# Performance work log

Measured on AMD Instinct MI355X. Metric: run time of the kernel, lower is better.

The kernel has to match this reference:

```python
import jax, jax.numpy as jnp
import numpy as np

D_MODEL = 768
N_HEADS = 12
HEAD_DIM = D_MODEL // N_HEADS
B, L = 2, 4096


def setup_inputs() -> dict:
    key = jax.random.key(0)
    ks = jax.random.split(key, 11)
    s = 0.02
    inp = {
        "q": jax.random.normal(ks[0], (B, L, D_MODEL), jnp.float32),
        "k": jax.random.normal(ks[1], (B, L, D_MODEL), jnp.float32),
        "v": jax.random.normal(ks[2], (B, L, D_MODEL), jnp.float32),
        # causal mask: True = masked (matches torch masked_fill semantics)
        "mask": jnp.triu(jnp.ones((L, L), bool), k=1)[None, None, :, :],
        "wq": jax.random.normal(ks[3], (D_MODEL, D_MODEL), jnp.float32) * s,
        "bq": jnp.zeros((D_MODEL,), jnp.float32),
        "wk": jax.random.normal(ks[4], (D_MODEL, D_MODEL), jnp.float32) * s,
        "bk": jnp.zeros((D_MODEL,), jnp.float32),
        "wv": jax.random.normal(ks[5], (D_MODEL, D_MODEL), jnp.float32) * s,
        "bv": jnp.zeros((D_MODEL,), jnp.float32),
        "wo": jax.random.normal(ks[6], (D_MODEL, D_MODEL), jnp.float32) * s,
        "bo": jnp.zeros((D_MODEL,), jnp.float32),
    }
    return inp


def reference(q, k, v, mask, wq, bq, wk, bk, wv, bv, wo, bo):
    Bs, Ls, Ds = q.shape

    def split_heads(x):  # [B,L,D] -> [B,H,L,hd]
        return x.reshape(Bs, -1, N_HEADS, HEAD_DIM).transpose(0, 2, 1, 3)

    qh = split_heads(q @ wq.T + bq)
    kh = split_heads(k @ wk.T + bk)
    vh = split_heads(v @ wv.T + bv)

    scores = jnp.einsum("bhqd,bhkd->bhqk", qh, kh) / jnp.sqrt(
        jnp.asarray(HEAD_DIM, qh.dtype)
    )
    scores = jnp.where(mask, -jnp.inf, scores)
    attn = jax.nn.softmax(scores, axis=-1)
    out = jnp.einsum("bhqk,bhkd->bhqd", attn, vh)  # [B,H,L,hd]
    out = out.transpose(0, 2, 1, 3).reshape(Bs, Ls, Ds)
    return out @ wo.T + bo
```

## Files before the change

### kernel.cpp

```cpp
#include <hip/hip_runtime.h>
#include <hip/hip_bf16.h>
#include <stdint.h>

#define DM 768
#define NH 12
#define HD 64
#define BB 2
#define LL 4096
#define BH (BB*NH)
#define ML (BB*LL)

typedef short bf16x8 __attribute__((ext_vector_type(8)));
typedef short bf16x4 __attribute__((ext_vector_type(4)));
typedef float f32x4 __attribute__((ext_vector_type(4)));

#define LOG2E 1.4426950408889634f

__device__ inline short f2b(float f) {
  __hip_bfloat16 h = __float2bfloat16(f);
  return *reinterpret_cast<short*>(&h);
}

__device__ inline void gll16(const void* g, void* l) {
  __builtin_amdgcn_global_load_lds(
      (const __attribute__((address_space(1))) unsigned int*)g,
      (__attribute__((address_space(3))) unsigned int*)l, 16, 0, 0);
}

__global__ __launch_bounds__(256) void convx_kernel(
    const float* __restrict__ src, short* __restrict__ dst)
{
  size_t i = ((size_t)blockIdx.x * 256 + threadIdx.x) * 8;
  float4 a = *(const float4*)(src + i);
  float4 b = *(const float4*)(src + i + 4);
  bf16x8 r = {f2b(a.x), f2b(a.y), f2b(a.z), f2b(a.w),
              f2b(b.x), f2b(b.y), f2b(b.z), f2b(b.w)};
  *(bf16x8*)(dst + i) = r;
}

__global__ __launch_bounds__(256) void convx3_kernel(
    const float* __restrict__ s0, const float* __restrict__ s1,
    const float* __restrict__ s2, short* __restrict__ d0,
    short* __restrict__ d1, short* __restrict__ d2)
{
  const float* src = blockIdx.y == 0 ? s0 : (blockIdx.y == 1 ? s1 : s2);
  short*       dst = blockIdx.y == 0 ? d0 : (blockIdx.y == 1 ? d1 : d2);
  size_t i = ((size_t)blockIdx.x * 256 + threadIdx.x) * 8;
  float4 a = *(const float4*)(src + i);
  float4 b = *(const float4*)(src + i + 4);
  bf16x8 r = {f2b(a.x), f2b(a.y), f2b(a.z), f2b(a.w),
              f2b(b.x), f2b(b.y), f2b(b.z), f2b(b.w)};
  *(bf16x8*)(dst + i) = r;
}

__global__ __launch_bounds__(256) void convw_kernel(
    const float* __restrict__ w0, const float* __restrict__ w1,
    const float* __restrict__ w2, const float* __restrict__ w3,
    short* __restrict__ o0, short* __restrict__ o1,
    short* __restrict__ o2, short* __restrict__ o3)
{
  const float* src; short* dst;
  switch (blockIdx.y) {
    case 0: src = w0; dst = o0; break;
    case 1: src = w1; dst = o1; break;
    case 2: src = w2; dst = o2; break;
    default: src = w3; dst = o3; break;
  }
  size_t i = ((size_t)blockIdx.x * 256 + threadIdx.x) * 8;
  float4 a = *(const float4*)(src + i);
  float4 b = *(const float4*)(src + i + 4);
  bf16x8 r = {f2b(a.x), f2b(a.y), f2b(a.z), f2b(a.w),
              f2b(b.x), f2b(b.y), f2b(b.z), f2b(b.w)};
  *(bf16x8*)(dst + i) = r;
}

__device__ __forceinline__ void gemm128_core(
    const short* __restrict__ A, const short* __restrict__ Bw,
    int m0, int n0, char* ab0, char* ab1, char* bb0, char* bb1,
    f32x4 (&acc)[4][4])
{
  const int lane   = threadIdx.x & 63;
  const int w      = threadIdx.x >> 6;
  const int g      = lane >> 4;
  const int mr     = lane & 15;
  const int wr     = w >> 1, wc = w & 1;
  const int srow   = lane >> 2;
  const int schunk = (lane & 3) ^ (srow & 3);
  const int rdswz  = (mr & 3) << 4;

  #pragma unroll
  for (int i = 0; i < 2; ++i) {
    gll16(A  + (size_t)(m0 + w * 32 + i * 16 + srow) * DM + schunk * 8,
          ab0 + (w * 32 + i * 16) * 64);
    gll16(Bw + (size_t)(n0 + w * 32 + i * 16 + srow) * DM + schunk * 8,
          bb0 + (w * 32 + i * 16) * 64);
  }

  const int nk = DM / 32;
  for (int t = 0; t < nk; ++t) {
    __syncthreads();
    if (t + 1 < nk) {
      const int k1 = (t + 1) * 32;
      char* an = ((t + 1) & 1) ? ab1 : ab0;
      char* bn = ((t + 1) & 1) ? bb1 : bb0;
      #pragma unroll
      for (int i = 0; i < 2; ++i) {
        gll16(A  + (size_t)(m0 + w * 32 + i * 16 + srow) * DM + k1 + schunk * 8,
              an + (w * 32 + i * 16) * 64);
        gll16(Bw + (size_t)(n0 + w * 32 + i * 16 + srow) * DM + k1 + schunk * 8,
              bn + (w * 32 + i * 16) * 64);
      }
    }
    const char* ac = (t & 1) ? ab1 : ab0;
    const char* bc = (t & 1) ? bb1 : bb0;
    bf16x8 af[4], bfr[4];
    #pragma unroll
    for (int m = 0; m < 4; ++m)
      af[m] = *(const bf16x8*)(ac + (wr * 64 + m * 16 + mr) * 64 + ((g * 16) ^ rdswz));
    #pragma unroll
    for (int n = 0; n < 4; ++n)
      bfr[n] = *(const bf16x8*)(bc + (wc * 64 + n * 16 + mr) * 64 + ((g * 16) ^ rdswz));
    #pragma unroll
    for (int m = 0; m < 4; ++m)
      #pragma unroll
      for (int n = 0; n < 4; ++n)
        acc[m][n] = __builtin_amdgcn_mfma_f32_16x16x32_bf16(af[m], bfr[n], acc[m][n], 0, 0, 0);
  }
}

__global__ __launch_bounds__(256) void qkv_gemm_kernel(
    const short* __restrict__ xq, const short* __restrict__ xk,
    const short* __restrict__ xv, const short* __restrict__ wqb,
    const short* __restrict__ wkb, const short* __restrict__ wvb,
    const float* __restrict__ bq, const float* __restrict__ bk,
    const float* __restrict__ bv, short* __restrict__ qh,
    short* __restrict__ kh, short* __restrict__ vt)
{
  __shared__ __align__(16) char abuf[2][128 * 64];
  __shared__ __align__(16) char bbuf[2][128 * 64];
  const int z = blockIdx.z;
  const short* A  = z == 0 ? xq : (z == 1 ? xk : xv);
  const short* Bw = z == 0 ? wqb : (z == 1 ? wkb : wvb);
  const float* bi = z == 0 ? bq : (z == 1 ? bk : bv);
  short* out      = z == 0 ? qh : (z == 1 ? kh : vt);
  const float scale = z == 0 ? 0.125f * LOG2E : 1.0f;
  const bool vmode  = (z == 2);
  const int m0 = blockIdx.x * 128;
  const int n0 = blockIdx.y * 128;

  f32x4 acc[4][4] = {};
  gemm128_core(A, Bw, m0, n0, abuf[0], abuf[1], bbuf[0], bbuf[1], acc);

  const int lane = threadIdx.x & 63;
  const int w    = threadIdx.x >> 6;
  const int g    = lane >> 4;
  const int mr   = lane & 15;
  const int wr   = w >> 1, wc = w & 1;
  #pragma unroll
  for (int nf = 0; nf < 4; ++nf) {
    const int col = n0 + wc * 64 + nf * 16 + mr;
    const float bv2 = bi[col];
    const int h = col >> 6, c = col & 63;
    #pragma unroll
    for (int m = 0; m < 4; ++m)
      #pragma unroll
      for (int r = 0; r < 4; ++r) {
        const int row = m0 + wr * 64 + m * 16 + g * 4 + r;
        const int b = row >> 12, li = row & 4095;
        const float val = (acc[m][nf][r] + bv2) * scale;
        size_t idx;
        if (vmode) idx = ((size_t)(b * NH + h) * HD + c) * LL + li;
        else       idx = ((size_t)(b * NH + h) * LL + li) * HD + c;
        out[idx] = f2b(val);
      }
  }
}

template<int MODE>
__global__ __launch_bounds__(256) void proj_gemm_kernel(
    const short* __restrict__ A, const short* __restrict__ Bw,
    const float* __restrict__ bias, short* __restrict__ out, float scale)
{
  __shared__ __align__(16) char abuf[2][128 * 64];
  __shared__ __align__(16) char bbuf[2][128 * 64];
  const int m0 = blockIdx.x * 128;
  const int n0 = blockIdx.y * 128;
  f32x4 acc[4][4] = {};
  gemm128_core(A, Bw, m0, n0, abuf[0], abuf[1], bbuf[0], bbuf[1], acc);

  const int lane = threadIdx.x & 63;
  const int w    = threadIdx.x >> 6;
  const int g    = lane >> 4;
  const int mr   = lane & 15;
  const int wr   = w >> 1, wc = w & 1;
  #pragma unroll
  for (int nf = 0; nf < 4; ++nf) {
    const int col = n0 + wc * 64 + nf * 16 + mr;
    const float bv = bias[col];
    const int h = col >> 6, c = col & 63;
    #pragma unroll
    for (int m = 0; m < 4; ++m)
      #pragma unroll
      for (int r = 0; r < 4; ++r) {
        const int row = m0 + wr * 64 + m * 16 + g * 4 + r;
        const int b = row >> 12, li = row & 4095;
        const float val = (acc[m][nf][r] + bv) * scale;
        size_t idx;
        if (MODE == 2) idx = ((size_t)(b * NH + h) * HD + c) * LL + li;
        else           idx = ((size_t)(b * NH + h) * LL + li) * HD + c;
        out[idx] = f2b(val);
      }
  }
}

__global__ __launch_bounds__(256) void outproj_kernel(
    const short* __restrict__ A, const short* __restrict__ Bw,
    const float* __restrict__ bias, float* __restrict__ out)
{
  __shared__ __align__(16) char abuf[2][128 * 64];
  __shared__ __align__(16) char bbuf[2][128 * 64];
  const int m0 = blockIdx.x * 128;
  const int n0 = blockIdx.y * 128;
  f32x4 acc[4][4] = {};
  gemm128_core(A, Bw, m0, n0, abuf[0], abuf[1], bbuf[0], bbuf[1], acc);

  const int lane = threadIdx.x & 63;
  const int w    = threadIdx.x >> 6;
  const int g    = lane >> 4;
  const int mr   = lane & 15;
  const int wr   = w >> 1, wc = w & 1;
  #pragma unroll
  for (int nf = 0; nf < 4; ++nf) {
    const int col = n0 + wc * 64 + nf * 16 + mr;
    const float bv = bias[col];
    #pragma unroll
    for (int m = 0; m < 4; ++m)
      #pragma unroll
      for (int r = 0; r < 4; ++r) {
        const int row = m0 + wr * 64 + m * 16 + g * 4 + r;
        out[(size_t)row * DM + col] = acc[m][nf][r] + bv;
      }
  }
}

__global__ __launch_bounds__(256) void attn_kernel(
    const short* __restrict__ qh, const short* __restrict__ kh,
    const short* __restrict__ vt, short* __restrict__ attn_out)
{
  __shared__ __align__(16) char kbuf[2][8192];
  __shared__ __align__(16) char vbuf[2][8192];
  __shared__ __align__(16) char plds[4][2048];

  const int bh   = blockIdx.y;
  const int lane = threadIdx.x & 63;
  const int w    = threadIdx.x >> 6;
  const int g    = lane >> 4;
  const int mr   = lane & 15;

  const short* qp = qh + (size_t)bh * LL * HD;
  const short* kp = kh + (size_t)bh * LL * HD;
  const short* vp = vt + (size_t)bh * HD * LL;
  char* wbase = plds[w];

  int wroff[4], rdoff[2];
  #pragma unroll
  for (int mf = 0; mf < 4; ++mf)
    wroff[mf] = mr * 128 + ((mf * 32 + g * 8) ^ ((mr & 7) << 4));
  #pragma unroll
  for (int c = 0; c < 2; ++c)
    rdoff[c] = mr * 128 + ((c * 64 + g * 16) ^ ((mr & 7) << 4));
  const int swz = (mr & 7) << 4;
  const int ssub = lane >> 3;
  const int scol = ((lane & 7) ^ ssub) * 8;

  const int b = bh / NH, h = bh % NH;

  #pragma unroll
  for (int ph = 0; ph < 2; ++ph) {
    const int qtile = ph == 0 ? (63 - (int)blockIdx.x) : (int)blockIdx.x;
    const int q0blk = qtile * 64;
    const int q0w   = q0blk + w * 16;
    const int nt    = qtile + 1;

    if (ph == 1) __syncthreads();

    const short* qrow = qp + (size_t)(q0w + mr) * HD + g * 8;
    bf16x8 qb0 = *(const bf16x8*)qrow;
    bf16x8 qb1 = *(const bf16x8*)(qrow + 32);

    f32x4 acc[4] = {};
    f32x4 lsum = {0.f, 0.f, 0.f, 0.f};

    #pragma unroll
    for (int p = 0; p < 2; ++p) {
      const int row = p * 32 + w * 8 + ssub;
      gll16(kp + (size_t)row * HD + scol, kbuf[0] + p * 4096 + w * 1024);
      gll16(vp + (size_t)row * LL + scol, vbuf[0] + p * 4096 + w * 1024);
    }

    for (int t = 0; t < nt; ++t) {
      __syncthreads();
      const int kv0 = t * 64;

      if (t + 1 < nt) {
        const int kv1 = kv0 + 64;
        char* kb = kbuf[(t + 1) & 1];
        char* vb = vbuf[(t + 1) & 1];
        #pragma unroll
        for (int p = 0; p < 2; ++p) {
          const int row = p * 32 + w * 8 + ssub;
          gll16(kp + (size_t)(kv1 + row) * HD + scol, kb + p * 4096 + w * 1024);
          gll16(vp + (size_t)row * LL + kv1 + scol, vb + p * 4096 + w * 1024);
        }
      }

      {
        const char* kb = kbuf[t & 1];
        const char* vb = vbuf[t & 1];

        f32x4 s[4] = {};
        #pragma unroll
        for (int mf = 0; mf < 4; ++mf) {
          const char* krow = kb + (mf * 16 + mr) * 128;
          bf16x8 ka0 = *(const bf16x8*)(krow + ((g * 16) ^ swz));
          bf16x8 ka1 = *(const bf16x8*)(krow + ((64 + g * 16) ^ swz));
          s[mf] = __builtin_amdgcn_mfma_f32_16x16x32_bf16(ka0, qb0, s[mf], 0, 0, 0);
          s[mf] = __builtin_amdgcn_mfma_f32_16x16x32_bf16(ka1, qb1, s[mf], 0, 0, 0);
        }

        if (kv0 + 63 > q0w) {
          #pragma unroll
          for (int mf = 0; mf < 4; ++mf)
            #pragma unroll
            for (int r = 0; r < 4; ++r)
              if (kv0 + mf * 16 + g * 4 + r > q0w + mr)
                s[mf][r] = -INFINITY;
        }

        #pragma unroll
        for (int mf = 0; mf < 4; ++mf) {
          #pragma unroll
          for (int r = 0; r < 4; ++r)
            s[mf][r] = exp2f(s[mf][r]);
          lsum += s[mf];
        }

        #pragma unroll
        for (int mf = 0; mf < 4; ++mf) {
          bf16x4 w4 = {f2b(s[mf][0]), f2b(s[mf][1]), f2b(s[mf][2]), f2b(s[mf][3])};
          *(bf16x4*)(wbase + wroff[mf]) = w4;
        }

        #pragma unroll
        for (int c = 0; c < 2; ++c) {
          bf16x8 pb = *(const bf16x8*)(wbase + rdoff[c]);
          #pragma unroll
          for (int df = 0; df < 4; ++df) {
            const char* vrow = vb + (df * 16 + mr) * 128;
            bf16x8 av = *(const bf16x8*)(vrow + ((c * 64 + g * 16) ^ swz));
            acc[df] = __builtin_amdgcn_mfma_f32_16x16x32_bf16(av, pb, acc[df], 0, 0, 0);
          }
        }
      }
    }

    float lreg = (lsum[0] + lsum[1]) + (lsum[2] + lsum[3]);
    lreg += __shfl_xor(lreg, 16, 64);
    lreg += __shfl_xor(lreg, 32, 64);

    const float inv = 1.0f / lreg;
    const int q = q0w + mr;
    short* orow = attn_out + ((size_t)(b * LL + q)) * DM + h * HD + g * 4;
    #pragma unroll
    for (int df = 0; df < 4; ++df) {
      bf16x4 st = {f2b(acc[df][0] * inv), f2b(acc[df][1] * inv),
                   f2b(acc[df][2] * inv), f2b(acc[df][3] * inv)};
      *(bf16x4*)(orow + df * 16) = st;
    }
  }
}

extern "C" void kernel_launch(void* const* d_in, const int* in_sizes, int n_in,
                              void* d_out, int out_size, void* d_ws, size_t ws_size,
                              hipStream_t stream) {
  const float* q  = (const float*)d_in[0];
  const float* k  = (const float*)d_in[1];
  const float* v  = (const float*)d_in[2];
  const float* wq = (const float*)d_in[4];
  const float* bq = (const float*)d_in[5];
  const float* wk = (const float*)d_in[6];
  const float* bk = (const float*)d_in[7];
  const float* wv = (const float*)d_in[8];
  const float* bv = (const float*)d_in[9];
  const float* wo = (const float*)d_in[10];
  const float* bo = (const float*)d_in[11];

  const size_t S   = (size_t)BH * LL * HD;
  const size_t WSZ = (size_t)DM * DM;
  short* qh   = (short*)d_ws;
  short* kh   = qh + S;
  short* vt   = kh + S;
  short* attn = vt + S;
  short* wqb  = attn + S;
  short* wkb  = wqb + WSZ;
  short* wvb  = wkb + WSZ;
  short* wob  = wvb + WSZ;
  short* xtra = wob + WSZ;

  const size_t need_fused = (size_t)(6 * S + 4 * WSZ) * sizeof(short);
  const bool fused = ws_size >= need_fused;

  dim3 blk(256);
  convw_kernel<<<dim3(WSZ / 2048, 4), blk, 0, stream>>>(wq, wk, wv, wo, wqb, wkb, wvb, wob);
  dim3 ggemm(ML / 128, DM / 128);

  if (fused) {
    short* xbq = attn;
    short* xbk = xtra;
    short* xbv = xtra + S;
    convx3_kernel<<<dim3(S / 2048, 3), blk, 0, stream>>>(q, k, v, xbq, xbk, xbv);
    qkv_gemm_kernel<<<dim3(ML / 128, DM / 128, 3), blk, 0, stream>>>(
        xbq, xbk, xbv, wqb, wkb, wvb, bq, bk, bv, qh, kh, vt);
  } else {
    short* xb = attn;
    convx_kernel<<<dim3(S / 2048), blk, 0, stream>>>(q, xb);
    proj_gemm_kernel<0><<<ggemm, blk, 0, stream>>>(xb, wqb, bq, qh, 0.125f * LOG2E);
    convx_kernel<<<dim3(S / 2048), blk, 0, stream>>>(k, xb);
    proj_gemm_kernel<1><<<ggemm, blk, 0, stream>>>(xb, wkb, bk, kh, 1.0f);
    convx_kernel<<<dim3(S / 2048), blk, 0, stream>>>(v, xb);
    proj_gemm_kernel<2><<<ggemm, blk, 0, stream>>>(xb, wvb, bv, vt, 1.0f);
  }

  attn_kernel<<<dim3(32, BH), blk, 0, stream>>>(qh, kh, vt, attn);
  outproj_kernel<<<ggemm, blk, 0, stream>>>(attn, wob, bo, (float*)d_out);
}
```

Measured before the change: 366.4 us.

## Vectorize GEMM epilogue stores via operand swap, merge conversions, remap attention blocks

The Q/K projection and output projection GEMMs swap operands so the accumulator's four consecutive values run along the feature dimension, which lets the epilogue write bf16x4 / float4 vectors in place of scalar strided stores. The V projection keeps its orientation but packs four consecutive tokens into one bf16x4 store in the transposed layout. The weight and activation fp32→bf16 conversions are merged into one kernel launch, and attention blocks are remapped so adjacent blocks share heads in groups of 8, aiming at better L2 locality for K/V. This removes scattered 2-byte stores and one launch, at the cost of more index arithmetic and changed tile mapping.

After: 361.3 us. About the same (-1.4%).

```diff
diff --git a/kernel.cpp b/kernel.cpp
--- a/kernel.cpp
+++ b/kernel.cpp
@@ -27,6 +27,34 @@
       (__attribute__((address_space(3))) unsigned int*)l, 16, 0, 0);
 }
 
+__global__ __launch_bounds__(256) void convall_kernel(
+    const float* __restrict__ q, const float* __restrict__ k,
+    const float* __restrict__ v, const float* __restrict__ wq,
+    const float* __restrict__ wk, const float* __restrict__ wv,
+    const float* __restrict__ wo, short* __restrict__ xq,
+    short* __restrict__ xk, short* __restrict__ xv,
+    short* __restrict__ wqb, short* __restrict__ wkb,
+    short* __restrict__ wvb, short* __restrict__ wob)
+{
+  const int b = blockIdx.x;
+  const float* src; short* dst; int base;
+  if (b < 9216) {
+    const int z = b / 3072; base = b % 3072;
+    src = z == 0 ? q : (z == 1 ? k : v);
+    dst = z == 0 ? xq : (z == 1 ? xk : xv);
+  } else {
+    const int b2 = b - 9216; const int z = b2 / 288; base = b2 % 288;
+    src = z == 0 ? wq : (z == 1 ? wk : (z == 2 ? wv : wo));
+    dst = z == 0 ? wqb : (z == 1 ? wkb : (z == 2 ? wvb : wob));
+  }
+  size_t i = ((size_t)base * 256 + threadIdx.x) * 8;
+  float4 a = *(const float4*)(src + i);
+  float4 c = *(const float4*)(src + i + 4);
+  bf16x8 r = {f2b(a.x), f2b(a.y), f2b(a.z), f2b(a.w),
+              f2b(c.x), f2b(c.y), f2b(c.z), f2b(c.w)};
+  *(bf16x8*)(dst + i) = r;
+}
+
 __global__ __launch_bounds__(256) void convx_kernel(
     const float* __restrict__ src, short* __restrict__ dst)
 {
@@ -37,22 +65,6 @@
               f2b(b.x), f2b(b.y), f2b(b.z), f2b(b.w)};
   *(bf16x8*)(dst + i) = r;
 }
-
-__global__ __launch_bounds__(256) void convx3_kernel(
-    const float* __restrict__ s0, const float* __restrict__ s1,
-    const float* __restrict__ s2, short* __restrict__ d0,
-    short* __restrict__ d1, short* __restrict__ d2)
-{
-  const float* src = blockIdx.y == 0 ? s0 : (blockIdx.y == 1 ? s1 : s2);
-  short*       dst = blockIdx.y == 0 ? d0 : (blockIdx.y == 1 ? d1 : d2);
-  size_t i = ((size_t)blockIdx.x * 256 + threadIdx.x) * 8;
-  float4 a = *(const float4*)(src + i);
-  float4 b = *(const float4*)(src + i + 4);
-  bf16x8 r = {f2b(a.x), f2b(a.y), f2b(a.z), f2b(a.w),
-              f2b(b.x), f2b(b.y), f2b(b.z), f2b(b.w)};
-  *(bf16x8*)(dst + i) = r;
-}
-
 __global__ __launch_bounds__(256) void convw_kernel(
     const float* __restrict__ w0, const float* __restrict__ w1,
     const float* __restrict__ w2, const float* __restrict__ w3,
@@ -128,6 +140,59 @@
   }
 }
 
+template<int Z>
+__device__ __forceinline__ void proj_body(
+    const short* __restrict__ X, const short* __restrict__ W,
+    const float* __restrict__ bi, short* __restrict__ out,
+    char* ab0, char* ab1, char* bb0, char* bb1, int bx, int by)
+{
+  const int lane = threadIdx.x & 63;
+  const int w    = threadIdx.x >> 6;
+  const int g    = lane >> 4;
+  const int mr   = lane & 15;
+  const int wr   = w >> 1, wc = w & 1;
+  f32x4 acc[4][4] = {};
+
+  if (Z == 2) {
+    const int m0 = bx * 128, n0 = by * 128;
+    gemm128_core(X, W, m0, n0, ab0, ab1, bb0, bb1, acc);
+    #pragma unroll
+    for (int nf = 0; nf < 4; ++nf) {
+      const int col = n0 + wc * 64 + nf * 16 + mr;
+      const float bv = bi[col];
+      const int h = col >> 6, c = col & 63;
+      #pragma unroll
+      for (int mf = 0; mf < 4; ++mf) {
+        const int tok0 = m0 + wr * 64 + mf * 16 + g * 4;
+        const int b = tok0 >> 12, li0 = tok0 & 4095;
+        bf16x4 st = {f2b(acc[mf][nf][0] + bv), f2b(acc[mf][nf][1] + bv),
+                     f2b(acc[mf][nf][2] + bv), f2b(acc[mf][nf][3] + bv)};
+        *(bf16x4*)(out + ((size_t)(b * NH + h) * HD + c) * LL + li0) = st;
+      }
+    }
+  } else {
+    const int m0 = by * 128, n0 = bx * 128;
+    gemm128_core(W, X, m0, n0, ab0, ab1, bb0, bb1, acc);
+    const float scale = (Z == 0) ? 0.125f * LOG2E : 1.0f;
+    #pragma unroll
+    for (int nf = 0; nf < 4; ++nf) {
+      const int tok = n0 + wc * 64 + nf * 16 + mr;
+      const int b = tok >> 12, li = tok & 4095;
+      #pragma unroll
+      for (int mf = 0; mf < 4; ++mf) {
+        const int feat0 = m0 + wr * 64 + mf * 16 + g * 4;
+        const int h = feat0 >> 6, c0 = feat0 & 63;
+        float4 bv4 = *(const float4*)(bi + feat0);
+        bf16x4 st = {f2b((acc[mf][nf][0] + bv4.x) * scale),
+                     f2b((acc[mf][nf][1] + bv4.y) * scale),
+                     f2b((acc[mf][nf][2] + bv4.z) * scale),
+                     f2b((acc[mf][nf][3] + bv4.w) * scale)};
+        *(bf16x4*)(out + ((size_t)(b * NH + h) * LL + li) * HD + c0) = st;
+      }
+    }
+  }
+}
+
 __global__ __launch_bounds__(256) void qkv_gemm_kernel(
     const short* __restrict__ xq, const short* __restrict__ xk,
     const short* __restrict__ xv, const short* __restrict__ wqb,
@@ -139,17 +204,38 @@
   __shared__ __align__(16) char abuf[2][128 * 64];
   __shared__ __align__(16) char bbuf[2][128 * 64];
   const int z = blockIdx.z;
-  const short* A  = z == 0 ? xq : (z == 1 ? xk : xv);
-  const short* Bw = z == 0 ? wqb : (z == 1 ? wkb : wvb);
-  const float* bi = z == 0 ? bq : (z == 1 ? bk : bv);
-  short* out      = z == 0 ? qh : (z == 1 ? kh : vt);
-  const float scale = z == 0 ? 0.125f * LOG2E : 1.0f;
-  const bool vmode  = (z == 2);
-  const int m0 = blockIdx.x * 128;
-  const int n0 = blockIdx.y * 128;
-
+  if (z == 0)
+    proj_body<0>(xq, wqb, bq, qh, abuf[0], abuf[1], bbuf[0], bbuf[1],
+                 blockIdx.x, blockIdx.y);
+  else if (z == 1)
+    proj_body<1>(xk, wkb, bk, kh, abuf[0], abuf[1], bbuf[0], bbuf[1],
+                 blockIdx.x, blockIdx.y);
+  else
+    proj_body<2>(xv, wvb, bv, vt, abuf[0], abuf[1], bbuf[0], bbuf[1],
+                 blockIdx.x, blockIdx.y);
+}
+
+template<int Z>
+__global__ __launch_bounds__(256) void proj1_kernel(
+    const short* __restrict__ X, const short* __restrict__ W,
+    const float* __restrict__ bi, short* __restrict__ out)
+{
+  __shared__ __align__(16) char abuf[2][128 * 64];
+  __shared__ __align__(16) char bbuf[2][128 * 64];
+  proj_body<Z>(X, W, bi, out, abuf[0], abuf[1], bbuf[0], bbuf[1],
+               blockIdx.x, blockIdx.y);
+}
+
+__global__ __launch_bounds__(256) void outproj_kernel(
+    const short* __restrict__ A, const short* __restrict__ Wb,
+    const float* __restrict__ bias, float* __restrict__ out)
+{
+  __shared__ __align__(16) char abuf[2][128 * 64];
+  __shared__ __align__(16) char bbuf[2][128 * 64];
+  const int m0 = blockIdx.y * 128;
+  const int n0 = blockIdx.x * 128;
   f32x4 acc[4][4] = {};
-  gemm128_core(A, Bw, m0, n0, abuf[0], abuf[1], bbuf[0], bbuf[1], acc);
+  gemm128_core(Wb, A, m0, n0, abuf[0], abuf[1], bbuf[0], bbuf[1], acc);
 
   const int lane = threadIdx.x & 63;
   const int w    = threadIdx.x >> 6;
@@ -158,88 +244,15 @@
   const int wr   = w >> 1, wc = w & 1;
   #pragma unroll
   for (int nf = 0; nf < 4; ++nf) {
-    const int col = n0 + wc * 64 + nf * 16 + mr;
-    const float bv2 = bi[col];
-    const int h = col >> 6, c = col & 63;
-    #pragma unroll
-    for (int m = 0; m < 4; ++m)
-      #pragma unroll
-      for (int r = 0; r < 4; ++r) {
-        const int row = m0 + wr * 64 + m * 16 + g * 4 + r;
-        const int b = row >> 12, li = row & 4095;
-        const float val = (acc[m][nf][r] + bv2) * scale;
-        size_t idx;
-        if (vmode) idx = ((size_t)(b * NH + h) * HD + c) * LL + li;
-        else       idx = ((size_t)(b * NH + h) * LL + li) * HD + c;
-        out[idx] = f2b(val);
-      }
-  }
-}
-
-template<int MODE>
-__global__ __launch_bounds__(256) void proj_gemm_kernel(
-    const short* __restrict__ A, const short* __restrict__ Bw,
-    const float* __restrict__ bias, short* __restrict__ out, float scale)
-{
-  __shared__ __align__(16) char abuf[2][128 * 64];
-  __shared__ __align__(16) char bbuf[2][128 * 64];
-  const int m0 = blockIdx.x * 128;
-  const int n0 = blockIdx.y * 128;
-  f32x4 acc[4][4] = {};
-  gemm128_core(A, Bw, m0, n0, abuf[0], abuf[1], bbuf[0], bbuf[1], acc);
-
-  const int lane = threadIdx.x & 63;
-  const int w    = threadIdx.x >> 6;
-  const int g    = lane >> 4;
-  const int mr   = lane & 15;
-  const int wr   = w >> 1, wc = w & 1;
-  #pragma unroll
-  for (int nf = 0; nf < 4; ++nf) {
-    const int col = n0 + wc * 64 + nf * 16 + mr;
-    const float bv = bias[col];
-    const int h = col >> 6, c = col & 63;
-    #pragma unroll
-    for (int m = 0; m < 4; ++m)
-      #pragma unroll
-      for (int r = 0; r < 4; ++r) {
-        const int row = m0 + wr * 64 + m * 16 + g * 4 + r;
-        const int b = row >> 12, li = row & 4095;
-        const float val = (acc[m][nf][r] + bv) * scale;
-        size_t idx;
-        if (MODE == 2) idx = ((size_t)(b * NH + h) * HD + c) * LL + li;
-        else           idx = ((size_t)(b * NH + h) * LL + li) * HD + c;
-        out[idx] = f2b(val);
-      }
-  }
-}
-
-__global__ __launch_bounds__(256) void outproj_kernel(
-    const short* __restrict__ A, const short* __restrict__ Bw,
-    const float* __restrict__ bias, float* __restrict__ out)
-{
-  __shared__ __align__(16) char abuf[2][128 * 64];
-  __shared__ __align__(16) char bbuf[2][128 * 64];
-  const int m0 = blockIdx.x * 128;
-  const int n0 = blockIdx.y * 128;
-  f32x4 acc[4][4] = {};
-  gemm128_core(A, Bw, m0, n0, abuf[0], abuf[1], bbuf[0], bbuf[1], acc);
-
-  const int lane = threadIdx.x & 63;
-  const int w    = threadIdx.x >> 6;
-  const int g    = lane >> 4;
-  const int mr   = lane & 15;
-  const int wr   = w >> 1, wc = w & 1;
-  #pragma unroll
-  for (int nf = 0; nf < 4; ++nf) {
-    const int col = n0 + wc * 64 + nf * 16 + mr;
-    const float bv = bias[col];
-    #pragma unroll
-    for (int m = 0; m < 4; ++m)
-      #pragma unroll
-      for (int r = 0; r < 4; ++r) {
-        const int row = m0 + wr * 64 + m * 16 + g * 4 + r;
-        out[(size_t)row * DM + col] = acc[m][nf][r] + bv;
-      }
+    const int tok = n0 + wc * 64 + nf * 16 + mr;
+    #pragma unroll
+    for (int mf = 0; mf < 4; ++mf) {
+      const int feat0 = m0 + wr * 64 + mf * 16 + g * 4;
+      float4 bv4 = *(const float4*)(bias + feat0);
+      float4 st = {acc[mf][nf][0] + bv4.x, acc[mf][nf][1] + bv4.y,
+                   acc[mf][nf][2] + bv4.z, acc[mf][nf][3] + bv4.w};
+      *(float4*)(out + (size_t)tok * DM + feat0) = st;
+    }
   }
 }
 
@@ -251,7 +264,10 @@
   __shared__ __align__(16) char vbuf[2][8192];
   __shared__ __align__(16) char plds[4][2048];
 
-  const int bh   = blockIdx.y;
+  const int d   = (int)blockIdx.y * 32 + (int)blockIdx.x;
+  const int bh  = (d & 7) + 8 * ((d >> 3) >> 5);
+  const int qi  = (d >> 3) & 31;
+
   const int lane = threadIdx.x & 63;
   const int w    = threadIdx.x >> 6;
   const int g    = lane >> 4;
@@ -277,7 +293,7 @@
 
   #pragma unroll
   for (int ph = 0; ph < 2; ++ph) {
-    const int qtile = ph == 0 ? (63 - (int)blockIdx.x) : (int)blockIdx.x;
+    const int qtile = ph == 0 ? (63 - qi) : qi;
     const int q0blk = qtile * 64;
     const int q0w   = q0blk + w * 16;
     const int nt    = qtile + 1;
@@ -411,24 +427,25 @@
   const bool fused = ws_size >= need_fused;
 
   dim3 blk(256);
-  convw_kernel<<<dim3(WSZ / 2048, 4), blk, 0, stream>>>(wq, wk, wv, wo, wqb, wkb, wvb, wob);
   dim3 ggemm(ML / 128, DM / 128);
 
   if (fused) {
     short* xbq = attn;
     short* xbk = xtra;
     short* xbv = xtra + S;
-    convx3_kernel<<<dim3(S / 2048, 3), blk, 0, stream>>>(q, k, v, xbq, xbk, xbv);
+    convall_kernel<<<dim3(3 * (S / 2048) + 4 * (WSZ / 2048)), blk, 0, stream>>>(
+        q, k, v, wq, wk, wv, wo, xbq, xbk, xbv, wqb, wkb, wvb, wob);
     qkv_gemm_kernel<<<dim3(ML / 128, DM / 128, 3), blk, 0, stream>>>(
         xbq, xbk, xbv, wqb, wkb, wvb, bq, bk, bv, qh, kh, vt);
   } else {
+    convw_kernel<<<dim3(WSZ / 2048, 4), blk, 0, stream>>>(wq, wk, wv, wo, wqb, wkb, wvb, wob);
     short* xb = attn;
     convx_kernel<<<dim3(S / 2048), blk, 0, stream>>>(q, xb);
-    proj_gemm_kernel<0><<<ggemm, blk, 0, stream>>>(xb, wqb, bq, qh, 0.125f * LOG2E);
+    proj1_kernel<0><<<ggemm, blk, 0, stream>>>(xb, wqb, bq, qh);
     convx_kernel<<<dim3(S / 2048), blk, 0, stream>>>(k, xb);
-    proj_gemm_kernel<1><<<ggemm, blk, 0, stream>>>(xb, wkb, bk, kh, 1.0f);
+    proj1_kernel<1><<<ggemm, blk, 0, stream>>>(xb, wkb, bk, kh);
     convx_kernel<<<dim3(S / 2048), blk, 0, stream>>>(v, xb);
-    proj_gemm_kernel<2><<<ggemm, blk, 0, stream>>>(xb, wvb, bv, vt, 1.0f);
+    proj1_kernel<2><<<ggemm, blk, 0, stream>>>(xb, wvb, bv, vt);
   }
 
   attn_kernel<<<dim3(32, BH), blk, 0, stream>>>(qh, kh, vt, attn);
```
